# Performance work log

Measured on AMD Instinct MI355X. Metric: run time of the kernel, lower is better.

The kernel has to match this reference:

```python
import jax, jax.numpy as jnp
import numpy as np

DT = 600.0          # integration time step (s)
STEPS = 20          # number of Euler steps
R_EARTH = 6371000.0
DEG2RAD = np.pi / 180.0
KERNEL = jnp.array([[1.0, 2.0, 1.0], [2.0, 4.0, 2.0], [1.0, 2.0, 1.0]], dtype=jnp.float32) / 16.0


def setup_inputs() -> dict:
    key = jax.random.key(0)
    kT, ku, kv, km = jax.random.split(key, 4)
    B, H, W = 8, 360, 720  # 0.5-degree global grid
    T = jax.random.normal(kT, (B, H, W), dtype=jnp.float32)
    ug = jax.random.normal(ku, (B, H, W), dtype=jnp.float32) * 0.5
    vg = jax.random.normal(kv, (B, H, W), dtype=jnp.float32) * 0.5
    lat = (90.0 - 0.25 - jnp.arange(H, dtype=jnp.float32) * 0.5)
    lon = jnp.arange(W, dtype=jnp.float32) * 0.5
    mask = (jax.random.uniform(km, (H, W)) > 0.3).astype(jnp.float32)  # ocean mask
    return {"T": T, "ug": ug, "vg": vg, "lat": lat, "lon": lon, "mask": mask}


def _horizontal_filter(field, mask):
    # field: (B, H, W); 3x3 binomial smoothing, zero ('valid'-style) padding=1, then mask
    k = KERNEL.reshape(1, 1, 3, 3).astype(field.dtype)
    f = jax.lax.conv_general_dilated(field[:, None, :, :], k, window_strides=(1, 1),
                                     padding=((1, 1), (1, 1)))
    return f[:, 0] * mask


def reference(T, ug, vg, lat, lon, mask):
    B, H, W = T.shape
    dlat = lat[1] - lat[0]
    dlon = lon[1] - lon[0]
    dy = R_EARTH * DEG2RAD * jnp.abs(dlat)
    sign_y = jnp.where(dlat > 0, 1.0, -1.0).astype(T.dtype)
    # dx varies with latitude: (H, 1) broadcasts over (B, H, W)
    dx = (R_EARTH * DEG2RAD * dlon) * jnp.cos(lat * DEG2RAD)[:, None]
    maskb = mask[None, :, :]

    def step(Tc, _):
        # boundary-aware meridional derivative
        top = (Tc[:, 1:2, :] - Tc[:, 0:1, :]) / dy
        bot = (Tc[:, -1:, :] - Tc[:, -2:-1, :]) / dy
        mid = (Tc[:, 2:, :] - Tc[:, :-2, :]) / (2.0 * dy)
        dT_dy = jnp.concatenate([top, mid, bot], axis=1) * sign_y
        # periodic zonal derivative
        dT_dx = (jnp.roll(Tc, -1, axis=2) - jnp.roll(Tc, 1, axis=2)) / (2.0 * dx)
        advection = ug * dT_dx + vg * dT_dy
        Tn = Tc - DT * advection * maskb  # Euler update with F = -advection*mask
        Tn = _horizontal_filter(Tn, maskb)
        return Tn, None

    T_final, _ = jax.lax.scan(step, T, None, length=STEPS)
    return T_final
```

## Files before the change

kernel.cpp:

```cpp
#include <hip/hip_runtime.h>

#define H 360
#define W 720
#define NB 8
#define TX 120
#define TY 45
#define GX 6
#define GY 8
#define LST 132
#define DTS 600.0f
#define REARTH 6371000.0f
#define D2R 0.017453292519943295f

#define ROWS_T 53
#define NQ1 (ROWS_T*32)
#define NHALO 346
#define NPAIRS 10
#define FLAG_STRIDE 32

static __device__ __forceinline__ float2 ldc8(const float* p) {
    unsigned long long u = __hip_atomic_load((const unsigned long long*)p,
                                             __ATOMIC_RELAXED, __HIP_MEMORY_SCOPE_AGENT);
    return __builtin_bit_cast(float2, u);
}
static __device__ __forceinline__ void stc8(float* p, float2 v) {
    __hip_atomic_store((unsigned long long*)p, __builtin_bit_cast(unsigned long long, v),
                       __ATOMIC_RELAXED, __HIP_MEMORY_SCOPE_AGENT);
}

__global__ __launch_bounds__(256, 2) void ocean_persist(
    const float* __restrict__ Tin, const float* __restrict__ ug,
    const float* __restrict__ vg, const float* __restrict__ lat,
    const float* __restrict__ lon, const float* __restrict__ mask,
    float* __restrict__ out, float* __restrict__ wsf, int* __restrict__ flags)
{
    __shared__ float sT[ROWS_T * LST];
    __shared__ float sHB[14 * LST];

    const int tid = threadIdx.x;
    const int b  = blockIdx.z;
    const int bx = blockIdx.x * TX;
    const int by = blockIdx.y * TY;
    const int plane = H * W;

    const float dlat = lat[1] - lat[0];
    const float dy   = REARTH * D2R * fabsf(dlat);
    const float sgn  = (dlat > 0.f) ? 1.f : -1.f;
    const float dlon = lon[1] - lon[0];
    const float i2dy = 0.5f / dy, i1dy = 1.f / dy;

    const float* Tb = Tin + b * plane;
    const float* ub = ug  + b * plane;
    const float* vb = vg  + b * plane;
    float* outb = out + b * plane;
    float* wsb  = wsf + b * plane;

    int* bflags = flags + b * (GX * GY) * FLAG_STRIDE;
    int* myflag = bflags + (blockIdx.y * GX + blockIdx.x) * FLAG_STRIDE;

    const int cq = tid & 31;
    const int rg = tid >> 5;
    const int c0 = cq << 2;
    const int a  = 1 + 7 * rg;
    const int cnt = (rg < 7) ? 7 : 2;
    const int gj0 = (bx - 4 + c0 + W) % W;
    const bool hlzb = (gj0 == 0);
    const bool hrzb = (gj0 + 3 == W - 1);
    const bool topB = (blockIdx.y == 0), botB = (blockIdx.y == GY - 1);

    int goff1[7], lds1o[7];
    #pragma unroll
    for (int k = 0; k < 7; ++k) {
        const int q = tid + 256 * k;
        if (q < NQ1) {
            const int r = q >> 5, cc0 = (q & 31) << 2;
            int gi = by - 4 + r; gi = min(max(gi, 0), H - 1);
            const int gj = (bx - 4 + cc0 + W) % W;
            goff1[k] = gi * W + gj;
            lds1o[k] = r * LST + cc0;
        } else goff1[k] = -1;
    }

    int hgo[2], hlo[2];
    #pragma unroll
    for (int t = 0; t < 2; ++t) {
        const int q = tid + 256 * t;
        if (q < NHALO) {
            int r, cc0;
            if (q < 256) { const int ri = q >> 5; r = (ri < 4) ? ri : 45 + ri; cc0 = (q & 31) << 2; }
            else { const int u = q - 256; r = 4 + (u >> 1); cc0 = (u & 1) ? 124 : 0; }
            int gi = by - 4 + r; gi = min(max(gi, 0), H - 1);
            const int gj = (bx - 4 + cc0 + W) % W;
            hgo[t] = gi * W + gj;
            hlo[t] = r * LST + cc0;
        } else hgo[t] = -1;
    }

    float cuA[7][4], cvA[7][4];
    unsigned domm = 0;
    #pragma unroll
    for (int j = 0; j < 7; ++j) {
        #pragma unroll
        for (int t = 0; t < 4; ++t) { cuA[j][t] = 0.f; cvA[j][t] = 0.f; }
        if (j < cnt) {
            const int gi = by - 4 + a + j;
            if ((unsigned)gi < H) {
                const float dxv  = REARTH * D2R * dlon * cosf(lat[gi] * D2R);
                const float rdx2 = 0.5f / dxv;
                const float ivy  = (gi == 0 || gi == H - 1) ? i1dy : i2dy;
                #pragma unroll
                for (int t = 0; t < 4; ++t) {
                    const int off = gi * W + gj0 + t;
                    const float mk = mask[off];
                    cuA[j][t] = -DTS * mk * ub[off] * rdx2;
                    cvA[j][t] = -DTS * mk * vb[off] * sgn * ivy;
                }
                domm |= 1u << j;
            }
        }
    }

    float m16A[7][4];
    int o3A[7];
    unsigned tilem = 0, ringm = 0;
    #pragma unroll
    for (int i = 0; i < 7; ++i) {
        #pragma unroll
        for (int t = 0; t < 4; ++t) m16A[i][t] = 0.f;
        o3A[i] = 0;
        if (rg < 7) {
            const int n = 2 + 7 * rg + i;
            const int gi = by - 4 + n;
            if ((unsigned)gi < H) {
                #pragma unroll
                for (int t = 0; t < 4; ++t)
                    m16A[i][t] = mask[gi * W + gj0 + t] * (1.f / 16.f);
            }
            const bool inTile = (n >= 4 && n <= 48 && cq >= 1 && cq <= 30);
            if (inTile) {
                o3A[i] = gi * W + bx + c0 - 4;
                tilem |= 1u << i;
                if (n <= 7 || n >= 45 || cq == 1 || cq == 30) ringm |= 1u << i;
            }
        }
    }

    const int* nbrF = myflag;
    if (tid < 8) {
        int dyn, dxn;
        if (tid < 3)      { dyn = -1; dxn = tid - 1; }
        else if (tid == 3){ dyn = 0;  dxn = -1; }
        else if (tid == 4){ dyn = 0;  dxn = 1; }
        else              { dyn = 1;  dxn = tid - 6; }
        const int ny = (int)blockIdx.y + dyn;
        const int nx = ((int)blockIdx.x + dxn + GX) % GX;
        if (ny >= 0 && ny < GY) nbrF = bflags + (ny * GX + nx) * FLAG_STRIDE;
    }

    #pragma unroll
    for (int k = 0; k < 7; ++k)
        if (goff1[k] >= 0)
            *(float4*)(sT + lds1o[k]) = *(const float4*)(Tb + goff1[k]);
    __syncthreads();

    auto substep = [&](bool isA, bool writeST, float* rcur, bool finalOut) {
        float4 hA[7];
        float4 m1 = *(const float4*)(sT + (a - 1) * LST + c0);
        float4 cc = *(const float4*)(sT + a * LST + c0);
        #pragma unroll
        for (int j = 0; j < 7; ++j) {
            if (j < cnt) {
                const float4 vU = m1, vC = cc;
                const float4 vD = *(const float4*)(sT + (a + j + 1) * LST + c0);
                const float tl = __shfl_up(vC.w, 1);
                const float tr = __shfl_down(vC.x, 1);
                const bool dj = (domm >> j) & 1;
                float4 o;
                o.x = (dj ? vC.x : 0.f) + cuA[j][0]*(vC.y - tl)   + cvA[j][0]*(vD.x - vU.x);
                o.y = (dj ? vC.y : 0.f) + cuA[j][1]*(vC.z - vC.x) + cvA[j][1]*(vD.y - vU.y);
                o.z = (dj ? vC.z : 0.f) + cuA[j][2]*(vC.w - vC.y) + cvA[j][2]*(vD.z - vU.z);
                o.w = (dj ? vC.w : 0.f) + cuA[j][3]*(tr   - vC.z) + cvA[j][3]*(vD.w - vU.w);
                float hl = __shfl_up(o.w, 1);
                float hr = __shfl_down(o.x, 1);
                if (hlzb) hl = 0.f;
                if (hrzb) hr = 0.f;
                hA[j].x = hl  + 2.f * o.x + o.y;
                hA[j].y = o.x + 2.f * o.y + o.z;
                hA[j].z = o.y + 2.f * o.z + o.w;
                hA[j].w = o.z + 2.f * o.w + hr;
                m1 = cc; cc = vD;
            }
        }
        if (rg >= 1) {
            *(float4*)(sHB + ((rg - 1) * 2)     * LST + c0) = hA[0];
            *(float4*)(sHB + ((rg - 1) * 2 + 1) * LST + c0) = hA[1];
        }
        __syncthreads();
        if (rg < 7) {
            const float4 hb0 = *(const float4*)(sHB + (2 * rg)     * LST + c0);
            const float4 hb1 = *(const float4*)(sHB + (2 * rg + 1) * LST + c0);
            float4 sA = {0,0,0,0}, sB = {0,0,0,0};
            #pragma unroll
            for (int i = 0; i < 7; ++i) {
                const float4 hm = hA[i];
                const float4 hc = (i < 6) ? hA[i + 1] : hb0;
                const float4 hp = (i < 5) ? hA[i + 2] : ((i == 5) ? hb0 : hb1);
                float4 o;
                o.x = (hm.x + 2.f * hc.x + hp.x) * m16A[i][0];
                o.y = (hm.y + 2.f * hc.y + hp.y) * m16A[i][1];
                o.z = (hm.z + 2.f * hc.z + hp.z) * m16A[i][2];
                o.w = (hm.w + 2.f * hc.w + hp.w) * m16A[i][3];
                if (writeST) *(float4*)(sT + (2 + 7 * rg + i) * LST + c0) = o;
                if (isA && i == 2) sA = o;
                if (isA && i == 4) sB = o;
                if (rcur && ((ringm >> i) & 1)) {
                    float2 lo; lo.x = o.x; lo.y = o.y;
                    float2 hi; hi.x = o.z; hi.y = o.w;
                    stc8(rcur + o3A[i], lo);
                    stc8(rcur + o3A[i] + 2, hi);
                }
                if (finalOut && ((tilem >> i) & 1))
                    *(float4*)(outb + o3A[i]) = o;
            }
            if (isA && topB && rg == 0) *(float4*)(sT + 3 * LST + c0)  = sA;
            if (isA && botB && rg == 6) *(float4*)(sT + 49 * LST + c0) = sB;
        }
        __syncthreads();
    };

    #pragma unroll 1
    for (int p = 0; p < NPAIRS; ++p) {
        if (p) {
            __syncthreads();
            if (tid == 0)
                __hip_atomic_store(myflag, p, __ATOMIC_RELAXED, __HIP_MEMORY_SCOPE_AGENT);
            if (tid < 64) {
                long long t0 = (long long)clock64();
                for (;;) {
                    const int v = (tid < 8)
                        ? __hip_atomic_load(nbrF, __ATOMIC_RELAXED, __HIP_MEMORY_SCOPE_AGENT)
                        : 0x7fffffff;
                    if (__all(v >= p)) break;
                    __builtin_amdgcn_s_sleep(1);
                    if ((long long)clock64() - t0 > 200000000LL) break;
                }
            }
            __syncthreads();
            const float* prev = ((p - 1) & 1) ? outb : wsb;
            #pragma unroll
            for (int t = 0; t < 2; ++t) {
                if (hgo[t] >= 0) {
                    const float2 lo = ldc8(prev + hgo[t]);
                    const float2 hi = ldc8(prev + hgo[t] + 2);
                    float4 v; v.x = lo.x; v.y = lo.y; v.z = hi.x; v.w = hi.y;
                    *(float4*)(sT + hlo[t]) = v;
                }
            }
            __syncthreads();
        }

        const bool last = (p == NPAIRS - 1);
        float* rcur = (p & 1) ? outb : wsb;
        substep(true,  true,       nullptr,             false);
        substep(false, !last,      last ? nullptr : rcur, last);
    }
}

extern "C" void kernel_launch(void* const* d_in, const int* in_sizes, int n_in,
                              void* d_out, int out_size, void* d_ws, size_t ws_size,
                              hipStream_t stream)
{
    const float* T    = (const float*)d_in[0];
    const float* ug   = (const float*)d_in[1];
    const float* vg   = (const float*)d_in[2];
    const float* lat  = (const float*)d_in[3];
    const float* lon  = (const float*)d_in[4];
    const float* mask = (const float*)d_in[5];
    float* out = (float*)d_out;

    int*   flags = (int*)d_ws;
    float* wsf   = (float*)((char*)d_ws + 65536);

    hipMemsetAsync(d_ws, 0, 65536, stream);

    ocean_persist<<<dim3(GX, GY, NB), dim3(256), 0, stream>>>(
        T, ug, vg, lat, lon, mask, out, wsf, flags);
}
```

Before: 144.3 us.

## Use larger tiles with 8-row halos to sync every four substeps

Changes the persistent kernel's tiling from 120x45 tiles with a 4-cell halo (two substeps per neighbor exchange) to 240x36 tiles with an 8-cell halo (four substeps per exchange). Blocks grow to 512 threads, and the grid shrinks to 3x10x8. This removes the shared h-buffer exchange between row groups by making each thread's row window overlap. The aim is to halve the number of inter-block flag waits and global halo reloads. The cost is more redundant halo computation per tile, fewer blocks to spread over the CUs, and larger per-thread register arrays.

```diff
diff --git a/kernel.cpp b/kernel.cpp
--- a/kernel.cpp
+++ b/kernel.cpp
@@ -3,19 +3,20 @@
 #define H 360
 #define W 720
 #define NB 8
-#define TX 120
-#define TY 45
-#define GX 6
-#define GY 8
-#define LST 132
+#define XC 3
+#define YC 10
+#define TX 240
+#define TY 36
+#define BPB (XC*YC)
+#define WR 52
+#define LST 260
 #define DTS 600.0f
 #define REARTH 6371000.0f
 #define D2R 0.017453292519943295f
 
-#define ROWS_T 53
-#define NQ1 (ROWS_T*32)
-#define NHALO 346
-#define NPAIRS 10
+#define NQ1 (WR*64)
+#define NHALO 1168
+#define NGROUPS 5
 #define FLAG_STRIDE 32
 
 static __device__ __forceinline__ float2 ldc8(const float* p) {
@@ -28,14 +29,13 @@
                        __ATOMIC_RELAXED, __HIP_MEMORY_SCOPE_AGENT);
 }
 
-__global__ __launch_bounds__(256, 2) void ocean_persist(
+__global__ __launch_bounds__(512, 2) void ocean_persist(
     const float* __restrict__ Tin, const float* __restrict__ ug,
     const float* __restrict__ vg, const float* __restrict__ lat,
     const float* __restrict__ lon, const float* __restrict__ mask,
     float* __restrict__ out, float* __restrict__ wsf, int* __restrict__ flags)
 {
-    __shared__ float sT[ROWS_T * LST];
-    __shared__ float sHB[14 * LST];
+    __shared__ float sT[WR * LST];
 
     const int tid = threadIdx.x;
     const int b  = blockIdx.z;
@@ -55,93 +55,86 @@
     float* outb = out + b * plane;
     float* wsb  = wsf + b * plane;
 
-    int* bflags = flags + b * (GX * GY) * FLAG_STRIDE;
-    int* myflag = bflags + (blockIdx.y * GX + blockIdx.x) * FLAG_STRIDE;
-
-    const int cq = tid & 31;
-    const int rg = tid >> 5;
+    int* bflags = flags + b * BPB * FLAG_STRIDE;
+    int* myflag = bflags + (blockIdx.y * XC + blockIdx.x) * FLAG_STRIDE;
+
+    const int cq = tid & 63;
+    const int rg = tid >> 6;
     const int c0 = cq << 2;
-    const int a  = 1 + 7 * rg;
-    const int cnt = (rg < 7) ? 7 : 2;
-    const int gj0 = (bx - 4 + c0 + W) % W;
+    const int a  = 1 + 6 * rg;
+    const int gj0 = (bx - 8 + c0 + W) % W;
     const bool hlzb = (gj0 == 0);
     const bool hrzb = (gj0 + 3 == W - 1);
-    const bool topB = (blockIdx.y == 0), botB = (blockIdx.y == GY - 1);
+    const bool topB = (blockIdx.y == 0), botB = (blockIdx.y == YC - 1);
 
     int goff1[7], lds1o[7];
     #pragma unroll
     for (int k = 0; k < 7; ++k) {
-        const int q = tid + 256 * k;
+        const int q = tid + 512 * k;
         if (q < NQ1) {
-            const int r = q >> 5, cc0 = (q & 31) << 2;
-            int gi = by - 4 + r; gi = min(max(gi, 0), H - 1);
-            const int gj = (bx - 4 + cc0 + W) % W;
+            const int r = q >> 6, cc0 = (q & 63) << 2;
+            int gi = by - 8 + r; gi = min(max(gi, 0), H - 1);
+            const int gj = (bx - 8 + cc0 + W) % W;
             goff1[k] = gi * W + gj;
             lds1o[k] = r * LST + cc0;
         } else goff1[k] = -1;
     }
 
-    int hgo[2], hlo[2];
-    #pragma unroll
-    for (int t = 0; t < 2; ++t) {
-        const int q = tid + 256 * t;
+    int hgo[3], hlo[3];
+    #pragma unroll
+    for (int t = 0; t < 3; ++t) {
+        const int q = tid + 512 * t;
         if (q < NHALO) {
             int r, cc0;
-            if (q < 256) { const int ri = q >> 5; r = (ri < 4) ? ri : 45 + ri; cc0 = (q & 31) << 2; }
-            else { const int u = q - 256; r = 4 + (u >> 1); cc0 = (u & 1) ? 124 : 0; }
-            int gi = by - 4 + r; gi = min(max(gi, 0), H - 1);
-            const int gj = (bx - 4 + cc0 + W) % W;
+            if (q < 1024) { const int ri = q >> 6; r = (ri < 8) ? ri : 36 + ri; cc0 = (q & 63) << 2; }
+            else { const int u = q - 1024; r = 8 + (u >> 2); const int qi = u & 3;
+                   cc0 = (qi < 2) ? (qi << 2) : (248 + ((qi - 2) << 2)); }
+            int gi = by - 8 + r; gi = min(max(gi, 0), H - 1);
+            const int gj = (bx - 8 + cc0 + W) % W;
             hgo[t] = gi * W + gj;
             hlo[t] = r * LST + cc0;
         } else hgo[t] = -1;
     }
 
-    float cuA[7][4], cvA[7][4];
+    float cuA[8][4], cvA[8][4];
     unsigned domm = 0;
     #pragma unroll
-    for (int j = 0; j < 7; ++j) {
+    for (int j = 0; j < 8; ++j) {
         #pragma unroll
         for (int t = 0; t < 4; ++t) { cuA[j][t] = 0.f; cvA[j][t] = 0.f; }
-        if (j < cnt) {
-            const int gi = by - 4 + a + j;
-            if ((unsigned)gi < H) {
-                const float dxv  = REARTH * D2R * dlon * cosf(lat[gi] * D2R);
-                const float rdx2 = 0.5f / dxv;
-                const float ivy  = (gi == 0 || gi == H - 1) ? i1dy : i2dy;
-                #pragma unroll
-                for (int t = 0; t < 4; ++t) {
-                    const int off = gi * W + gj0 + t;
-                    const float mk = mask[off];
-                    cuA[j][t] = -DTS * mk * ub[off] * rdx2;
-                    cvA[j][t] = -DTS * mk * vb[off] * sgn * ivy;
-                }
-                domm |= 1u << j;
-            }
-        }
-    }
-
-    float m16A[7][4];
-    int o3A[7];
-    unsigned tilem = 0, ringm = 0;
-    #pragma unroll
-    for (int i = 0; i < 7; ++i) {
-        #pragma unroll
-        for (int t = 0; t < 4; ++t) m16A[i][t] = 0.f;
+        const int gi = by - 8 + a + j;
+        if ((unsigned)gi < H) {
+            const float dxv  = REARTH * D2R * dlon * cosf(lat[gi] * D2R);
+            const float rdx2 = 0.5f / dxv;
+            const float ivy  = (gi == 0 || gi == H - 1) ? i1dy : i2dy;
+            #pragma unroll
+            for (int t = 0; t < 4; ++t) {
+                const int off = gi * W + gj0 + t;
+                const float mk = mask[off];
+                cuA[j][t] = -DTS * mk * ub[off] * rdx2;
+                cvA[j][t] = -DTS * mk * vb[off] * sgn * ivy;
+            }
+            domm |= 1u << j;
+        }
+    }
+
+    float m16A[6][4];
+    int o3A[6];
+    unsigned outm = 0, tilem = 0, ringm = 0;
+    #pragma unroll
+    for (int i = 0; i < 6; ++i) {
+        const int n = 2 + 6 * rg + i;
+        const int gi = by - 8 + n;
         o3A[i] = 0;
-        if (rg < 7) {
-            const int n = 2 + 7 * rg + i;
-            const int gi = by - 4 + n;
-            if ((unsigned)gi < H) {
-                #pragma unroll
-                for (int t = 0; t < 4; ++t)
-                    m16A[i][t] = mask[gi * W + gj0 + t] * (1.f / 16.f);
-            }
-            const bool inTile = (n >= 4 && n <= 48 && cq >= 1 && cq <= 30);
-            if (inTile) {
-                o3A[i] = gi * W + bx + c0 - 4;
-                tilem |= 1u << i;
-                if (n <= 7 || n >= 45 || cq == 1 || cq == 30) ringm |= 1u << i;
-            }
+        #pragma unroll
+        for (int t = 0; t < 4; ++t)
+            m16A[i][t] = ((unsigned)gi < H) ? mask[gi * W + gj0 + t] * (1.f / 16.f) : 0.f;
+        if ((unsigned)gi < H) outm |= 1u << i;
+        const bool inTile = (n >= 8 && n <= 43 && cq >= 2 && cq <= 61);
+        if (inTile) {
+            o3A[i] = gi * W + bx + c0 - 8;
+            tilem |= 1u << i;
+            if (n <= 15 || n >= 36 || cq <= 3 || cq >= 60) ringm |= 1u << i;
         }
     }
 
@@ -153,8 +146,8 @@
         else if (tid == 4){ dyn = 0;  dxn = 1; }
         else              { dyn = 1;  dxn = tid - 6; }
         const int ny = (int)blockIdx.y + dyn;
-        const int nx = ((int)blockIdx.x + dxn + GX) % GX;
-        if (ny >= 0 && ny < GY) nbrF = bflags + (ny * GX + nx) * FLAG_STRIDE;
+        const int nx = ((int)blockIdx.x + dxn + XC) % XC;
+        if (ny >= 0 && ny < YC) nbrF = bflags + (ny * XC + nx) * FLAG_STRIDE;
     }
 
     #pragma unroll
@@ -163,92 +156,79 @@
             *(float4*)(sT + lds1o[k]) = *(const float4*)(Tb + goff1[k]);
     __syncthreads();
 
-    auto substep = [&](bool isA, bool writeST, float* rcur, bool finalOut) {
-        float4 hA[7];
+    auto substep = [&](bool finalOut, float* ring) {
+        float4 hA[8];
         float4 m1 = *(const float4*)(sT + (a - 1) * LST + c0);
         float4 cc = *(const float4*)(sT + a * LST + c0);
         #pragma unroll
-        for (int j = 0; j < 7; ++j) {
-            if (j < cnt) {
-                const float4 vU = m1, vC = cc;
-                const float4 vD = *(const float4*)(sT + (a + j + 1) * LST + c0);
-                const float tl = __shfl_up(vC.w, 1);
-                const float tr = __shfl_down(vC.x, 1);
-                const bool dj = (domm >> j) & 1;
-                float4 o;
-                o.x = (dj ? vC.x : 0.f) + cuA[j][0]*(vC.y - tl)   + cvA[j][0]*(vD.x - vU.x);
-                o.y = (dj ? vC.y : 0.f) + cuA[j][1]*(vC.z - vC.x) + cvA[j][1]*(vD.y - vU.y);
-                o.z = (dj ? vC.z : 0.f) + cuA[j][2]*(vC.w - vC.y) + cvA[j][2]*(vD.z - vU.z);
-                o.w = (dj ? vC.w : 0.f) + cuA[j][3]*(tr   - vC.z) + cvA[j][3]*(vD.w - vU.w);
-                float hl = __shfl_up(o.w, 1);
-                float hr = __shfl_down(o.x, 1);
-                if (hlzb) hl = 0.f;
-                if (hrzb) hr = 0.f;
-                hA[j].x = hl  + 2.f * o.x + o.y;
-                hA[j].y = o.x + 2.f * o.y + o.z;
-                hA[j].z = o.y + 2.f * o.z + o.w;
-                hA[j].w = o.z + 2.f * o.w + hr;
-                m1 = cc; cc = vD;
-            }
-        }
-        if (rg >= 1) {
-            *(float4*)(sHB + ((rg - 1) * 2)     * LST + c0) = hA[0];
-            *(float4*)(sHB + ((rg - 1) * 2 + 1) * LST + c0) = hA[1];
+        for (int j = 0; j < 8; ++j) {
+            const float4 vD = *(const float4*)(sT + (a + j + 1) * LST + c0);
+            const float tl = __shfl_up(cc.w, 1);
+            const float tr = __shfl_down(cc.x, 1);
+            const bool dj = (domm >> j) & 1;
+            float4 o;
+            o.x = (dj ? cc.x : 0.f) + cuA[j][0]*(cc.y - tl)   + cvA[j][0]*(vD.x - m1.x);
+            o.y = (dj ? cc.y : 0.f) + cuA[j][1]*(cc.z - cc.x) + cvA[j][1]*(vD.y - m1.y);
+            o.z = (dj ? cc.z : 0.f) + cuA[j][2]*(cc.w - cc.y) + cvA[j][2]*(vD.z - m1.z);
+            o.w = (dj ? cc.w : 0.f) + cuA[j][3]*(tr   - cc.z) + cvA[j][3]*(vD.w - m1.w);
+            float hl = __shfl_up(o.w, 1);
+            float hr = __shfl_down(o.x, 1);
+            if (hlzb) hl = 0.f;
+            if (hrzb) hr = 0.f;
+            hA[j].x = hl  + 2.f * o.x + o.y;
+            hA[j].y = o.x + 2.f * o.y + o.z;
+            hA[j].z = o.y + 2.f * o.z + o.w;
+            hA[j].w = o.z + 2.f * o.w + hr;
+            m1 = cc; cc = vD;
         }
         __syncthreads();
-        if (rg < 7) {
-            const float4 hb0 = *(const float4*)(sHB + (2 * rg)     * LST + c0);
-            const float4 hb1 = *(const float4*)(sHB + (2 * rg + 1) * LST + c0);
-            float4 sA = {0,0,0,0}, sB = {0,0,0,0};
-            #pragma unroll
-            for (int i = 0; i < 7; ++i) {
-                const float4 hm = hA[i];
-                const float4 hc = (i < 6) ? hA[i + 1] : hb0;
-                const float4 hp = (i < 5) ? hA[i + 2] : ((i == 5) ? hb0 : hb1);
-                float4 o;
-                o.x = (hm.x + 2.f * hc.x + hp.x) * m16A[i][0];
-                o.y = (hm.y + 2.f * hc.y + hp.y) * m16A[i][1];
-                o.z = (hm.z + 2.f * hc.z + hp.z) * m16A[i][2];
-                o.w = (hm.w + 2.f * hc.w + hp.w) * m16A[i][3];
-                if (writeST) *(float4*)(sT + (2 + 7 * rg + i) * LST + c0) = o;
-                if (isA && i == 2) sA = o;
-                if (isA && i == 4) sB = o;
-                if (rcur && ((ringm >> i) & 1)) {
-                    float2 lo; lo.x = o.x; lo.y = o.y;
-                    float2 hi; hi.x = o.z; hi.y = o.w;
-                    stc8(rcur + o3A[i], lo);
-                    stc8(rcur + o3A[i] + 2, hi);
-                }
-                if (finalOut && ((tilem >> i) & 1))
-                    *(float4*)(outb + o3A[i]) = o;
-            }
-            if (isA && topB && rg == 0) *(float4*)(sT + 3 * LST + c0)  = sA;
-            if (isA && botB && rg == 6) *(float4*)(sT + 49 * LST + c0) = sB;
+        #pragma unroll
+        for (int i = 0; i < 6; ++i) {
+            const float4 hm = hA[i], hc = hA[i + 1], hp = hA[i + 2];
+            float4 o;
+            o.x = (hm.x + 2.f * hc.x + hp.x) * m16A[i][0];
+            o.y = (hm.y + 2.f * hc.y + hp.y) * m16A[i][1];
+            o.z = (hm.z + 2.f * hc.z + hp.z) * m16A[i][2];
+            o.w = (hm.w + 2.f * hc.w + hp.w) * m16A[i][3];
+            if (!finalOut) {
+                if ((outm >> i) & 1)
+                    *(float4*)(sT + (2 + 6 * rg + i) * LST + c0) = o;
+                if (topB && rg == 1 && i == 0) *(float4*)(sT + 7  * LST + c0) = o;
+                if (botB && rg == 6 && i == 5) *(float4*)(sT + 44 * LST + c0) = o;
+            } else if ((tilem >> i) & 1) {
+                *(float4*)(outb + o3A[i]) = o;
+            }
+            if (ring && ((ringm >> i) & 1)) {
+                float2 lo; lo.x = o.x; lo.y = o.y;
+                float2 hi; hi.x = o.z; hi.y = o.w;
+                stc8(ring + o3A[i], lo);
+                stc8(ring + o3A[i] + 2, hi);
+            }
         }
         __syncthreads();
     };
 
     #pragma unroll 1
-    for (int p = 0; p < NPAIRS; ++p) {
-        if (p) {
+    for (int g = 0; g < NGROUPS; ++g) {
+        if (g) {
             __syncthreads();
             if (tid == 0)
-                __hip_atomic_store(myflag, p, __ATOMIC_RELAXED, __HIP_MEMORY_SCOPE_AGENT);
+                __hip_atomic_store(myflag, g, __ATOMIC_RELAXED, __HIP_MEMORY_SCOPE_AGENT);
             if (tid < 64) {
                 long long t0 = (long long)clock64();
                 for (;;) {
                     const int v = (tid < 8)
                         ? __hip_atomic_load(nbrF, __ATOMIC_RELAXED, __HIP_MEMORY_SCOPE_AGENT)
                         : 0x7fffffff;
-                    if (__all(v >= p)) break;
+                    if (__all(v >= g)) break;
                     __builtin_amdgcn_s_sleep(1);
                     if ((long long)clock64() - t0 > 200000000LL) break;
                 }
             }
             __syncthreads();
-            const float* prev = ((p - 1) & 1) ? outb : wsb;
+            const float* prev = ((g - 1) & 1) ? wsb : outb;
             #pragma unroll
-            for (int t = 0; t < 2; ++t) {
+            for (int t = 0; t < 3; ++t) {
                 if (hgo[t] >= 0) {
                     const float2 lo = ldc8(prev + hgo[t]);
                     const float2 hi = ldc8(prev + hgo[t] + 2);
@@ -258,11 +238,12 @@
             }
             __syncthreads();
         }
-
-        const bool last = (p == NPAIRS - 1);
-        float* rcur = (p & 1) ? outb : wsb;
-        substep(true,  true,       nullptr,             false);
-        substep(false, !last,      last ? nullptr : rcur, last);
+        const bool lastG = (g == NGROUPS - 1);
+        float* ring = lastG ? nullptr : ((g & 1) ? wsb : outb);
+        substep(false, nullptr);
+        substep(false, nullptr);
+        substep(false, nullptr);
+        substep(lastG, ring);
     }
 }
 
@@ -283,6 +264,6 @@
 
     hipMemsetAsync(d_ws, 0, 65536, stream);
 
-    ocean_persist<<<dim3(GX, GY, NB), dim3(256), 0, stream>>>(
+    ocean_persist<<<dim3(XC, YC, NB), dim3(512), 0, stream>>>(
         T, ug, vg, lat, lon, mask, out, wsf, flags);
 }
```

Result: faster. 141.2 us (-2.1%).
